# Kernel tuning notes

Measured on AMD Instinct MI355X. Metric: run time of the kernel, lower is better.

The kernel has to match this reference:

```python
import jax, jax.numpy as jnp
import numpy as np

B, T, D, H = 4, 2048, 1024, 16
HD = D // H  # 64

def setup_inputs() -> dict:
    key = jax.random.key(0)
    k1, k2, k3 = jax.random.split(key, 3)
    scale = 1.0 / np.sqrt(D)
    x = jax.random.normal(k1, (B, T, D), dtype=jnp.float32)
    w_qkv = jax.random.normal(k2, (D, 3 * D), dtype=jnp.float32) * scale
    w_o = jax.random.normal(k3, (D, D), dtype=jnp.float32) * scale
    return {"x": x, "w_qkv": w_qkv, "w_o": w_o}

def reference(x, w_qkv, w_o):
    b, t, d = x.shape
    qkv = jnp.einsum('btd,de->bte', x, w_qkv)  # [B,T,3D]
    q, k, v = jnp.split(qkv, 3, axis=-1)
    # [B,H,T,hd]
    q = q.reshape(b, t, H, HD).transpose(0, 2, 1, 3)
    k = k.reshape(b, t, H, HD).transpose(0, 2, 1, 3)
    v = v.reshape(b, t, H, HD).transpose(0, 2, 1, 3)
    scores = jnp.einsum('bhqd,bhkd->bhqk', q, k) * (1.0 / jnp.sqrt(jnp.asarray(HD, x.dtype)))
    causal = jnp.tril(jnp.ones((t, t), dtype=bool))
    scores = jnp.where(causal[None, None, :, :], scores, -jnp.inf)
    weights = jax.nn.softmax(scores, axis=-1)
    out = jnp.einsum('bhqk,bhkd->bhqd', weights, v)
    out = out.transpose(0, 2, 1, 3).reshape(b, t, d)
    return jnp.einsum('btd,de->bte', out, w_o)
```

## Files before the change

### kernel.cpp

```cpp
#include <hip/hip_runtime.h>
#include <hip/hip_bf16.h>
#include <stdint.h>

#define HD 64
#define NH 16
#define TT 2048
#define DD 1024

typedef uint16_t u16;
typedef __bf16 bf16_t;
typedef bf16_t bf16x8 __attribute__((ext_vector_type(8)));
typedef float f32x4 __attribute__((ext_vector_type(4)));

__device__ __forceinline__ u16 f2b(float f) {
    union { float f; uint32_t u; } v; v.f = f;
    uint32_t u = v.u;
    u += 0x7fff + ((u >> 16) & 1);
    return (u16)(u >> 16);
}

__device__ __forceinline__ u16 b16(float f) {
    union { __bf16 h; u16 u; } c; c.h = (__bf16)f; return c.u;
}

__device__ __forceinline__ float ex2(float x) { return __builtin_amdgcn_exp2f(x); }

__device__ __forceinline__ void gload16(const void* g, void* l) {
    __builtin_amdgcn_global_load_lds(
        (__attribute__((address_space(1))) void*)g,
        (__attribute__((address_space(3))) void*)l, 16, 0, 0);
}


__global__ void f32_to_bf16_vec(const float* __restrict__ in, u16* __restrict__ out, int n4) {
    int i = blockIdx.x * 256 + threadIdx.x;
    if (i >= n4) return;
    float4 v = ((const float4*)in)[i];
    ushort4 r;
    r.x = f2b(v.x); r.y = f2b(v.y); r.z = f2b(v.z); r.w = f2b(v.w);
    ((ushort4*)out)[i] = r;
}

__global__ void transpose_f32_bf16(const float* __restrict__ in, u16* __restrict__ out, int R, int C) {
    __shared__ float tile[32][33];
    const int tx = threadIdx.x, ty = threadIdx.y;
    const int c0 = blockIdx.x * 32, r0 = blockIdx.y * 32;
#pragma unroll
    for (int j = 0; j < 32; j += 8)
        tile[ty + j][tx] = in[(size_t)(r0 + ty + j) * C + c0 + tx];
    __syncthreads();
#pragma unroll
    for (int j = 0; j < 32; j += 8)
        out[(size_t)(c0 + ty + j) * R + r0 + tx] = f2b(tile[tx][ty + j]);
}


template<int MODE>
__global__ __launch_bounds__(512, 4)
void gemm9(const u16* __restrict__ A, const u16* __restrict__ Bt,
           int N, int K, int nwg,
           u16* __restrict__ oq, u16* __restrict__ ok, u16* __restrict__ ovT,
           float* __restrict__ of)
{
    __shared__ __align__(16) u16 As[3][256 * 32];
    __shared__ __align__(16) u16 Bs[3][128 * 32];
    const int tid = threadIdx.x;
    const int lane = tid & 63, l15 = lane & 15, g = lane >> 4;
    const int wid = tid >> 6, wm = wid >> 1, wn = wid & 1;

    const int gx = N >> 7;
    const int cpx = nwg >> 3;
    const int sid = (blockIdx.x & 7) * cpx + (blockIdx.x >> 3);
    const long row0 = (long)(sid / gx) * 256;
    const long col0 = (long)(sid % gx) * 128;

    const u16* Ag = A + row0 * K;
    const u16* Bg = Bt + col0 * K;

    const f32x4 z4 = {0.f, 0.f, 0.f, 0.f};
    f32x4 acc[4][4];
#pragma unroll
    for (int i = 0; i < 4; i++)
#pragma unroll
        for (int n = 0; n < 4; n++) acc[i][n] = z4;

    const int swz = (l15 >> 1) & 3;

#define STG(t_, s_) do { const int ko = (t_) << 5;                                                 \
        { const int c = tid;       const int r_ = c >> 2;                                          \
          gload16(Ag + (size_t)r_ * K + ko + ((((c & 3) ^ ((r_ >> 1) & 3))) << 3), &As[s_][c << 3]); } \
        { const int c = tid + 512; const int r_ = c >> 2;                                          \
          gload16(Ag + (size_t)r_ * K + ko + ((((c & 3) ^ ((r_ >> 1) & 3))) << 3), &As[s_][c << 3]); } \
        { const int c = tid;       const int r_ = c >> 2;                                          \
          gload16(Bg + (size_t)r_ * K + ko + ((((c & 3) ^ ((r_ >> 1) & 3))) << 3), &Bs[s_][c << 3]); } \
    } while (0)

    const int NT = K >> 5;
    STG(0, 0);
    STG(1, 1);
    int sc = 0;
    for (int t = 0; t < NT; ++t) {
        if (t < NT - 1) asm volatile("s_waitcnt vmcnt(3)" ::: "memory");
        else            asm volatile("s_waitcnt vmcnt(0)" ::: "memory");
        __builtin_amdgcn_s_barrier();
        bf16x8 af[4], bfr[4];
#pragma unroll
        for (int m = 0; m < 4; m++)
            af[m]  = *(const bf16x8*)&As[sc][(wm * 64 + m * 16 + l15) * 32 + ((g ^ swz) << 3)];
#pragma unroll
        for (int n = 0; n < 4; n++)
            bfr[n] = *(const bf16x8*)&Bs[sc][(wn * 64 + n * 16 + l15) * 32 + ((g ^ swz) << 3)];
        const int sn = (sc == 0) ? 2 : sc - 1;
        if (t + 2 < NT) STG(t + 2, sn);
        __builtin_amdgcn_s_setprio(1);
#pragma unroll
        for (int m = 0; m < 4; m++)
#pragma unroll
            for (int n = 0; n < 4; n++)
                acc[m][n] = __builtin_amdgcn_mfma_f32_16x16x32_bf16(af[m], bfr[n], acc[m][n], 0, 0, 0);
        __builtin_amdgcn_s_setprio(0);
        sc = (sc == 2) ? 0 : sc + 1;
    }
#undef STG

    if (MODE == 0) {
        const int which = (int)(col0 >> 10);
        const long b = row0 >> 11;
#pragma unroll
        for (int m = 0; m < 4; m++) {
            const long r = row0 + wm * 64 + m * 16 + g * 4;
            const long t = r & (TT - 1);
#pragma unroll
            for (int n = 0; n < 4; n++) {
                const long c = col0 + wn * 64 + n * 16 + l15;
                const int h  = (int)((c >> 6) & 15);
                const int hd = (int)(c & 63);
                if (which == 0) {
#pragma unroll
                    for (int e = 0; e < 4; e++)
                        oq[((b * NH + h) * TT + t + e) * HD + hd] = f2b(acc[m][n][e] * 0.18033688f);
                } else if (which == 1) {
#pragma unroll
                    for (int e = 0; e < 4; e++)
                        ok[((b * NH + h) * TT + t + e) * HD + hd] = f2b(acc[m][n][e]);
                } else {
                    ushort4 pk;
                    pk.x = f2b(acc[m][n][0]); pk.y = f2b(acc[m][n][1]);
                    pk.z = f2b(acc[m][n][2]); pk.w = f2b(acc[m][n][3]);
                    *(ushort4*)&ovT[((b * NH + h) * HD + hd) * TT + t] = pk;
                }
            }
        }
    } else {
#pragma unroll
        for (int m = 0; m < 4; m++) {
            const long r = row0 + wm * 64 + m * 16 + g * 4;
#pragma unroll
            for (int n = 0; n < 4; n++) {
                const long c = col0 + wn * 64 + n * 16 + l15;
#pragma unroll
                for (int e = 0; e < 4; e++)
                    of[(r + e) * (long)N + c] = acc[m][n][e];
            }
        }
    }
}


__global__ __launch_bounds__(256, 3)
void attn_fwd(const u16* __restrict__ gq, const u16* __restrict__ gk,
              const u16* __restrict__ gvT, u16* __restrict__ o)
{
    __shared__ __align__(16) u16 Klds[2][64 * 64];
    __shared__ __align__(16) u16 Vlds[2][64 * 64];
    __shared__ __align__(16) u16 Plds[4][32 * 64];

    const int tid = threadIdx.x;
    const int wv = tid >> 6, lane = tid & 63, l15 = lane & 15, g = lane >> 4;
    const int bh = blockIdx.x & 63;
    const int qt = 15 - (blockIdx.x >> 6);
    const int q0 = qt * 128;
    const int qw0 = q0 + wv * 32;

    const u16* qbase = gq + (size_t)bh * TT * HD;
    const u16* kbase = gk + (size_t)bh * TT * HD;
    const u16* vbase = gvT + (size_t)bh * HD * TT;

    const float NEG_INF = -__builtin_inff();
    const f32x4 z4 = {0.f, 0.f, 0.f, 0.f};

    bf16x8 qf[2][2];
#pragma unroll
    for (int qi = 0; qi < 2; qi++)
#pragma unroll
        for (int hs = 0; hs < 2; hs++)
            qf[qi][hs] = *(const bf16x8*)(qbase + (size_t)(qw0 + qi * 16 + l15) * HD + hs * 32 + g * 8);

    f32x4 o_acc[2][4];
    float m[2], ls[2];
#pragma unroll
    for (int qi = 0; qi < 2; qi++) {
#pragma unroll
        for (int n = 0; n < 4; n++) o_acc[qi][n] = z4;
        m[qi] = NEG_INF; ls[qi] = 0.f;
    }

    const int r0_ = tid >> 3, c0_ = tid & 7;
    const int r1_ = (tid + 256) >> 3, c1_ = (tid + 256) & 7;

#define STAGE(buf, k0s)                                                                    \
    do {                                                                                   \
        gload16(kbase + (size_t)((k0s) + r0_) * HD + ((c0_ ^ (r0_ & 7)) * 8), &Klds[buf][tid * 8]);          \
        gload16(kbase + (size_t)((k0s) + r1_) * HD + ((c1_ ^ (r1_ & 7)) * 8), &Klds[buf][(tid + 256) * 8]);  \
        gload16(vbase + (size_t)r0_ * TT + (k0s) + ((c0_ ^ (r0_ & 7)) * 8), &Vlds[buf][tid * 8]);            \
        gload16(vbase + (size_t)r1_ * TT + (k0s) + ((c1_ ^ (r1_ & 7)) * 8), &Vlds[buf][(tid + 256) * 8]);    \
    } while (0)

    const int nkt = q0 / 64 + 2;
    STAGE(0, 0);
    for (int kt = 0; kt < nkt; ++kt) {
        const int k0 = kt * 64;
        const int cur = kt & 1;
        if (kt + 1 < nkt) {
            STAGE(cur ^ 1, k0 + 64);
            asm volatile("s_waitcnt vmcnt(4)" ::: "memory");
        } else {
            asm volatile("s_waitcnt vmcnt(0)" ::: "memory");
        }
        __builtin_amdgcn_s_barrier();
        if (k0 <= qw0 + 31) {
            const int sw = l15 & 7;
            f32x4 s2[2][4];
            __builtin_amdgcn_s_setprio(1);
#pragma unroll
            for (int kb = 0; kb < 4; kb++) {
                bf16x8 kf0 = *(const bf16x8*)&Klds[cur][(kb * 16 + l15) * 64 + ((g ^ sw) * 8)];
                bf16x8 kf1 = *(const bf16x8*)&Klds[cur][(kb * 16 + l15) * 64 + (((4 + g) ^ sw) * 8)];
#pragma unroll
                for (int qi = 0; qi < 2; qi++) {
                    f32x4 t0 = __builtin_amdgcn_mfma_f32_16x16x32_bf16(kf0, qf[qi][0], z4, 0, 0, 0);
                    s2[qi][kb] = __builtin_amdgcn_mfma_f32_16x16x32_bf16(kf1, qf[qi][1], t0, 0, 0, 0);
                }
            }
            __builtin_amdgcn_s_setprio(0);
            if (k0 + 63 > qw0) {
#pragma unroll
                for (int qi = 0; qi < 2; qi++)
#pragma unroll
                    for (int kb = 0; kb < 4; kb++)
#pragma unroll
                        for (int e = 0; e < 4; e++) {
                            const int kk = k0 + kb * 16 + g * 4 + e;
                            const int qq = qw0 + qi * 16 + l15;
                            if (kk > qq) s2[qi][kb][e] = NEG_INF;
                        }
            }
#pragma unroll
            for (int qi = 0; qi < 2; qi++) {
                f32x4 mx = s2[qi][0];
#pragma unroll
                for (int kb = 1; kb < 4; kb++)
#pragma unroll
                    for (int e = 0; e < 4; e++) mx[e] = fmaxf(mx[e], s2[qi][kb][e]);
                float pmax = fmaxf(fmaxf(mx[0], mx[1]), fmaxf(mx[2], mx[3]));
                pmax = fmaxf(pmax, __shfl_xor(pmax, 16));
                pmax = fmaxf(pmax, __shfl_xor(pmax, 32));
                float mn = m[qi];
                const int resc = !__all(pmax <= mn + 11.541560f);
                if (resc) {
                    const float mold = mn;
                    mn = fmaxf(mold, pmax);
                    m[qi] = mn;
                    const float sc2 = ex2(mold - mn);
                    ls[qi] *= sc2;
#pragma unroll
                    for (int e = 0; e < 4; e++) {
                        const float sce = __shfl(sc2, (lane & 48) + (((lane >> 4) & 3) << 2) + e);
#pragma unroll
                        for (int n = 0; n < 4; n++) o_acc[qi][n][e] *= sce;
                    }
                }
                const int prow = qi * 16 + l15;
                u16* pb = &Plds[wv][prow * 64];
                float rsum = 0.f;
#pragma unroll
                for (int kb = 0; kb < 4; kb++) {
                    const float p0 = ex2(s2[qi][kb][0] - mn);
                    const float p1 = ex2(s2[qi][kb][1] - mn);
                    const float p2 = ex2(s2[qi][kb][2] - mn);
                    const float p3 = ex2(s2[qi][kb][3] - mn);
                    rsum += (p0 + p1) + (p2 + p3);
                    ushort4 pk;
                    pk.x = b16(p0); pk.y = b16(p1); pk.z = b16(p2); pk.w = b16(p3);
                    *(ushort4*)&pb[(((kb << 2) + g) ^ l15) * 4] = pk;
                }
                rsum += __shfl_xor(rsum, 16);
                rsum += __shfl_xor(rsum, 32);
                ls[qi] += rsum;
            }
            asm volatile("s_waitcnt lgkmcnt(0)" ::: "memory");
            const int sw2 = l15 & 7;
#pragma unroll
            for (int ks = 0; ks < 2; ks++) {
                bf16x8 vf[4];
#pragma unroll
                for (int n = 0; n < 4; n++)
                    vf[n] = *(const bf16x8*)&Vlds[cur][(n * 16 + l15) * 64 + (((ks * 4 + g) ^ sw2) * 8)];
                __builtin_amdgcn_s_setprio(1);
#pragma unroll
                for (int qi = 0; qi < 2; qi++) {
                    const u16* pb = &Plds[wv][(qi * 16 + l15) * 64];
                    const int G0 = ((ks << 3) + (g << 1)) ^ l15;
                    const int G1 = ((ks << 3) + (g << 1) + 1) ^ l15;
                    const uint2 ra = *(const uint2*)&pb[G0 * 4];
                    const uint2 rb = *(const uint2*)&pb[G1 * 4];
                    union { uint32_t w[4]; bf16x8 v; } pu;
                    pu.w[0] = ra.x; pu.w[1] = ra.y; pu.w[2] = rb.x; pu.w[3] = rb.y;
#pragma unroll
                    for (int n = 0; n < 4; n++)
                        o_acc[qi][n] = __builtin_amdgcn_mfma_f32_16x16x32_bf16(pu.v, vf[n], o_acc[qi][n], 0, 0, 0);
                }
                __builtin_amdgcn_s_setprio(0);
            }
        }
        __builtin_amdgcn_s_barrier();
    }
#undef STAGE

    const int b = bh >> 4, h = bh & 15;
#pragma unroll
    for (int qi = 0; qi < 2; qi++) {
        const float linv = 1.f / ls[qi];
#pragma unroll
        for (int e = 0; e < 4; e++) {
            const float inv = __shfl(linv, (lane & 48) + (((lane >> 4) & 3) << 2) + e);
            const int t = qw0 + qi * 16 + g * 4 + e;
#pragma unroll
            for (int n = 0; n < 4; n++)
                o[((size_t)(b * TT + t)) * DD + h * HD + n * 16 + l15] = b16(o_acc[qi][n][e] * inv);
        }
    }
}


extern "C" void kernel_launch(void* const* d_in, const int* in_sizes, int n_in,
                              void* d_out, int out_size, void* d_ws, size_t ws_size,
                              hipStream_t stream)
{
    const float* x     = (const float*)d_in[0];
    const float* w_qkv = (const float*)d_in[1];
    const float* w_o   = (const float*)d_in[2];
    float* out = (float*)d_out;
    char* ws = (char*)d_ws;

    u16* xb    = (u16*)(ws);
    u16* wqkvT = (u16*)(ws + 16777216);
    u16* woT   = (u16*)(ws + 23068672);
    u16* wsq   = (u16*)(ws + 25165824);
    u16* wsk   = (u16*)(ws + 41943040);
    u16* wsvT  = (u16*)(ws + 58720256);
    u16* attno = (u16*)(ws + 75497472);

    f32_to_bf16_vec<<<8192, 256, 0, stream>>>(x, xb, 2097152);
    dim3 tb(32, 8);
    transpose_f32_bf16<<<dim3(96, 32), tb, 0, stream>>>(w_qkv, wqkvT, 1024, 3072);
    transpose_f32_bf16<<<dim3(32, 32), tb, 0, stream>>>(w_o,   woT,   1024, 1024);

    gemm9<0><<<768, 512, 0, stream>>>(xb, wqkvT, 3072, 1024, 768, wsq, wsk, wsvT, nullptr);
    attn_fwd<<<1024, 256, 0, stream>>>(wsq, wsk, wsvT, attno);
    gemm9<1><<<256, 512, 0, stream>>>(attno, woT, 1024, 1024, 256, nullptr, nullptr, nullptr, out);
}
```

Before: 163.1 us.

## Shrink GEMM tile to 128x128 with K=64 stages and double buffering

The GEMM tile changes from 256x128 with K-step 32 and triple buffering to 128x128 with K-step 64 and double buffering. The LDS swizzle becomes an 8-way XOR, and each iteration issues two K sub-steps of MFMAs. Grid sizes double (1536 and 512 workgroups) to give more parallelism across CUs, especially for the small output projection. The trade-offs are lower arithmetic intensity per tile and a full vmcnt(0) wait every iteration, which shortens the load/compute overlap.

```diff
diff --git a/kernel.cpp b/kernel.cpp
--- a/kernel.cpp
+++ b/kernel.cpp
@@ -57,13 +57,13 @@
 
 template<int MODE>
 __global__ __launch_bounds__(512, 4)
-void gemm9(const u16* __restrict__ A, const u16* __restrict__ Bt,
-           int N, int K, int nwg,
-           u16* __restrict__ oq, u16* __restrict__ ok, u16* __restrict__ ovT,
-           float* __restrict__ of)
+void gemm10(const u16* __restrict__ A, const u16* __restrict__ Bt,
+            int N, int K, int nwg,
+            u16* __restrict__ oq, u16* __restrict__ ok, u16* __restrict__ ovT,
+            float* __restrict__ of)
 {
-    __shared__ __align__(16) u16 As[3][256 * 32];
-    __shared__ __align__(16) u16 Bs[3][128 * 32];
+    __shared__ __align__(16) u16 As[2][128 * 64];
+    __shared__ __align__(16) u16 Bs[2][128 * 64];
     const int tid = threadIdx.x;
     const int lane = tid & 63, l15 = lane & 15, g = lane >> 4;
     const int wid = tid >> 6, wm = wid >> 1, wn = wid & 1;
@@ -71,55 +71,57 @@
     const int gx = N >> 7;
     const int cpx = nwg >> 3;
     const int sid = (blockIdx.x & 7) * cpx + (blockIdx.x >> 3);
-    const long row0 = (long)(sid / gx) * 256;
+    const long row0 = (long)(sid / gx) * 128;
     const long col0 = (long)(sid % gx) * 128;
 
     const u16* Ag = A + row0 * K;
     const u16* Bg = Bt + col0 * K;
 
     const f32x4 z4 = {0.f, 0.f, 0.f, 0.f};
-    f32x4 acc[4][4];
-#pragma unroll
-    for (int i = 0; i < 4; i++)
+    f32x4 acc[2][4];
+#pragma unroll
+    for (int i = 0; i < 2; i++)
 #pragma unroll
         for (int n = 0; n < 4; n++) acc[i][n] = z4;
 
-    const int swz = (l15 >> 1) & 3;
-
-#define STG(t_, s_) do { const int ko = (t_) << 5;                                                 \
-        { const int c = tid;       const int r_ = c >> 2;                                          \
-          gload16(Ag + (size_t)r_ * K + ko + ((((c & 3) ^ ((r_ >> 1) & 3))) << 3), &As[s_][c << 3]); } \
-        { const int c = tid + 512; const int r_ = c >> 2;                                          \
-          gload16(Ag + (size_t)r_ * K + ko + ((((c & 3) ^ ((r_ >> 1) & 3))) << 3), &As[s_][c << 3]); } \
-        { const int c = tid;       const int r_ = c >> 2;                                          \
-          gload16(Bg + (size_t)r_ * K + ko + ((((c & 3) ^ ((r_ >> 1) & 3))) << 3), &Bs[s_][c << 3]); } \
+    const int sw = l15 & 7;
+
+#define STG(t_, s_) do { const int ko = (t_) << 6;                                                  \
+        { const int c = tid;       const int r_ = c >> 3;                                           \
+          gload16(Ag + (size_t)r_ * K + ko + (((c & 7) ^ (r_ & 7)) << 3), &As[s_][c << 3]); }       \
+        { const int c = tid + 512; const int r_ = c >> 3;                                           \
+          gload16(Ag + (size_t)r_ * K + ko + (((c & 7) ^ (r_ & 7)) << 3), &As[s_][c << 3]); }       \
+        { const int c = tid;       const int r_ = c >> 3;                                           \
+          gload16(Bg + (size_t)r_ * K + ko + (((c & 7) ^ (r_ & 7)) << 3), &Bs[s_][c << 3]); }       \
+        { const int c = tid + 512; const int r_ = c >> 3;                                           \
+          gload16(Bg + (size_t)r_ * K + ko + (((c & 7) ^ (r_ & 7)) << 3), &Bs[s_][c << 3]); }       \
     } while (0)
 
-    const int NT = K >> 5;
+    const int NT = K >> 6;
     STG(0, 0);
-    STG(1, 1);
-    int sc = 0;
     for (int t = 0; t < NT; ++t) {
-        if (t < NT - 1) asm volatile("s_waitcnt vmcnt(3)" ::: "memory");
-        else            asm volatile("s_waitcnt vmcnt(0)" ::: "memory");
+        const int cur = t & 1;
+        asm volatile("s_waitcnt vmcnt(0)" ::: "memory");
         __builtin_amdgcn_s_barrier();
-        bf16x8 af[4], bfr[4];
-#pragma unroll
-        for (int m = 0; m < 4; m++)
-            af[m]  = *(const bf16x8*)&As[sc][(wm * 64 + m * 16 + l15) * 32 + ((g ^ swz) << 3)];
-#pragma unroll
-        for (int n = 0; n < 4; n++)
-            bfr[n] = *(const bf16x8*)&Bs[sc][(wn * 64 + n * 16 + l15) * 32 + ((g ^ swz) << 3)];
-        const int sn = (sc == 0) ? 2 : sc - 1;
-        if (t + 2 < NT) STG(t + 2, sn);
-        __builtin_amdgcn_s_setprio(1);
-#pragma unroll
-        for (int m = 0; m < 4; m++)
+        if (t + 1 < NT) STG(t + 1, cur ^ 1);
+#pragma unroll
+        for (int ks = 0; ks < 2; ks++) {
+            bf16x8 af[2], bfr[4];
+            const int ce = ((ks * 4 + g) ^ sw) << 3;
+#pragma unroll
+            for (int m = 0; m < 2; m++)
+                af[m]  = *(const bf16x8*)&As[cur][(wm * 32 + m * 16 + l15) * 64 + ce];
 #pragma unroll
             for (int n = 0; n < 4; n++)
-                acc[m][n] = __builtin_amdgcn_mfma_f32_16x16x32_bf16(af[m], bfr[n], acc[m][n], 0, 0, 0);
-        __builtin_amdgcn_s_setprio(0);
-        sc = (sc == 2) ? 0 : sc + 1;
+                bfr[n] = *(const bf16x8*)&Bs[cur][(wn * 64 + n * 16 + l15) * 64 + ce];
+            __builtin_amdgcn_s_setprio(1);
+#pragma unroll
+            for (int m = 0; m < 2; m++)
+#pragma unroll
+                for (int n = 0; n < 4; n++)
+                    acc[m][n] = __builtin_amdgcn_mfma_f32_16x16x32_bf16(af[m], bfr[n], acc[m][n], 0, 0, 0);
+            __builtin_amdgcn_s_setprio(0);
+        }
     }
 #undef STG
 
@@ -127,8 +129,8 @@
         const int which = (int)(col0 >> 10);
         const long b = row0 >> 11;
 #pragma unroll
-        for (int m = 0; m < 4; m++) {
-            const long r = row0 + wm * 64 + m * 16 + g * 4;
+        for (int m = 0; m < 2; m++) {
+            const long r = row0 + wm * 32 + m * 16 + g * 4;
             const long t = r & (TT - 1);
 #pragma unroll
             for (int n = 0; n < 4; n++) {
@@ -153,8 +155,8 @@
         }
     } else {
 #pragma unroll
-        for (int m = 0; m < 4; m++) {
-            const long r = row0 + wm * 64 + m * 16 + g * 4;
+        for (int m = 0; m < 2; m++) {
+            const long r = row0 + wm * 32 + m * 16 + g * 4;
 #pragma unroll
             for (int n = 0; n < 4; n++) {
                 const long c = col0 + wn * 64 + n * 16 + l15;
@@ -366,7 +368,7 @@
     transpose_f32_bf16<<<dim3(96, 32), tb, 0, stream>>>(w_qkv, wqkvT, 1024, 3072);
     transpose_f32_bf16<<<dim3(32, 32), tb, 0, stream>>>(w_o,   woT,   1024, 1024);
 
-    gemm9<0><<<768, 512, 0, stream>>>(xb, wqkvT, 3072, 1024, 768, wsq, wsk, wsvT, nullptr);
+    gemm10<0><<<1536, 512, 0, stream>>>(xb, wqkvT, 3072, 1024, 1536, wsq, wsk, wsvT, nullptr);
     attn_fwd<<<1024, 256, 0, stream>>>(wsq, wsk, wsvT, attno);
-    gemm9<1><<<256, 512, 0, stream>>>(attno, woT, 1024, 1024, 256, nullptr, nullptr, nullptr, out);
-}
+    gemm10<1><<<512, 512, 0, stream>>>(attno, woT, 1024, 1024, 512, nullptr, nullptr, nullptr, out);
+}
```

Measured after the change: 157.8 us, median of 2. 3.2% less time.
